# Kernel tuning notes

Hardware: AMD Instinct MI355X
Metric: run time of the kernel (lower is better)

Reference implementation:

```python
import jax, jax.numpy as jnp
import numpy as np
import math

D_MODEL = 1024
D_NEURON = 4 * D_MODEL
B, T = 2, 4096


def setup_inputs() -> dict:
    key = jax.random.key(0)
    ks = jax.random.split(key, 8)
    s = 1.0 / math.sqrt(D_MODEL)
    so = 1.0 / math.sqrt(D_NEURON)
    x = jax.random.normal(ks[0], (B, T, D_MODEL), dtype=jnp.float32)
    W_main = jax.random.uniform(ks[1], (D_NEURON, D_MODEL), jnp.float32, -s, s)
    W_gate = jax.random.uniform(ks[2], (D_NEURON, D_MODEL), jnp.float32, -s, s)
    W_mod = jax.random.uniform(ks[3], (D_NEURON, D_MODEL), jnp.float32, -s, s)
    W_out = jax.random.uniform(ks[4], (D_MODEL, D_NEURON), jnp.float32, -so, so)
    W_delta = jax.random.uniform(ks[5], (D_NEURON, D_MODEL), jnp.float32, -s, s)
    b_delta = jnp.full((D_NEURON,), -3.0, dtype=jnp.float32)
    # S4-style init: A_log = linspace(log(0.001), log(0.1), d_neuron)
    A_log = jnp.linspace(math.log(0.001), math.log(0.1), D_NEURON).astype(jnp.float32)
    sw_logit = jnp.zeros((D_NEURON,), dtype=jnp.float32)  # inv_sigmoid(0.5) = 0
    state = jnp.zeros((B, D_NEURON), dtype=jnp.float32)
    return {"x": x, "state": state, "W_main": W_main, "W_gate": W_gate,
            "W_mod": W_mod, "W_out": W_out, "W_delta": W_delta,
            "b_delta": b_delta, "A_log": A_log, "sw_logit": sw_logit}


def reference(x, state, W_main, W_gate, W_mod, W_out, W_delta, b_delta, A_log, sw_logit):
    # x: [B,T,Dm]; all projections to d_neuron Dn = 4*Dm
    raw = jnp.einsum('btm,nm->btn', x, W_main)            # [B,T,Dn]
    gate = jax.nn.sigmoid(jnp.einsum('btm,nm->btn', x, W_gate))
    mod = jnp.tanh(jnp.einsum('btm,nm->btn', x, W_mod))
    delta = jax.nn.softplus(jnp.einsum('btm,nm->btn', x, W_delta) + b_delta)
    A = -jnp.exp(A_log)                                   # [Dn]
    decay_t = jnp.exp(delta * A)                          # [B,T,Dn]
    update = (1.0 - decay_t) * gate * jnp.tanh(raw)       # [B,T,Dn]

    def step(s, du):
        d, u = du
        s = d * s + u
        return s, s

    # scan over time axis; carry [B,Dn]
    final_state, all_states = jax.lax.scan(
        step, state,
        (jnp.swapaxes(decay_t, 0, 1), jnp.swapaxes(update, 0, 1)))
    all_states = jnp.swapaxes(all_states, 0, 1)           # [B,T,Dn]

    sw = jax.nn.sigmoid(sw_logit)
    mixed = (1.0 - sw) * jax.nn.gelu(raw, approximate=False) + sw * all_states
    out = jnp.einsum('btn,mn->btm', mixed * (1.0 + mod), W_out)  # [B,T,Dm]
    return out, jax.lax.stop_gradient(final_state)
```

## Files before the change

### kernel.cpp

```cpp
#include <hip/hip_runtime.h>
#include <hip/hip_bf16.h>
#include <stdint.h>

#define DM 1024
#define DN 4096
#define BB 2
#define TT 4096
#define MR (BB*TT)
#define TC 512
#define NTC (TT/TC)
#define CR (BB*TC)
#define CN ((size_t)CR*DN)
#define SCH 16

typedef unsigned short u16;
typedef __attribute__((ext_vector_type(8))) short bf16x8;
typedef __attribute__((ext_vector_type(4))) float f32x4;

__device__ __forceinline__ float bf2f(u16 u) {
    unsigned int x = ((unsigned int)u) << 16; float f; __builtin_memcpy(&f, &x, 4); return f;
}
__device__ __forceinline__ u16 f2bf(float f) {
    __hip_bfloat16 h = __float2bfloat16(f); u16 u; __builtin_memcpy(&u, &h, 2); return u;
}
__device__ __forceinline__ float tanh_fast(float x) {
    float e = __expf(2.f * x);
    return 1.f - 2.f / (e + 1.f);
}
__device__ __forceinline__ float erf_fast(float x) {
    float ax = fabsf(x);
    float t = 1.f / (1.f + 0.3275911f * ax);
    float y = t * (0.254829592f + t * (-0.284496736f + t * (1.421413741f +
              t * (-1.453152027f + t * 1.061405429f))));
    float r = 1.f - y * __expf(-ax * ax);
    return copysignf(r, x);
}
__device__ __forceinline__ void async16(const void* g, void* l) {
    __builtin_amdgcn_global_load_lds(
        (const __attribute__((address_space(1))) void*)(uintptr_t)g,
        (__attribute__((address_space(3))) void*)(uint32_t)(uintptr_t)l,
        16, 0, 0);
}

__global__ void cvt7_kernel(const float4* __restrict__ x,
                            const float4* __restrict__ w0, const float4* __restrict__ w1,
                            const float4* __restrict__ w2, const float4* __restrict__ w3,
                            const float4* __restrict__ wo, const float4* __restrict__ st,
                            ushort4* __restrict__ xb, ushort4* __restrict__ w4b,
                            ushort4* __restrict__ woutb, float4* __restrict__ state_cur)
{
    const int XQ = (MR * DM) / 4;
    const int WQ = (DN * DM) / 4;
    const int SQ = XQ + 5 * WQ;
    int i = blockIdx.x * 256 + threadIdx.x;
    if (i >= SQ) {
        int j = i - SQ;
        if (j < (BB * DN) / 4) state_cur[j] = st[j];
        return;
    }
    const float4* s; ushort4* d;
    if (i < XQ) { s = x + i; d = xb + i; }
    else {
        int j = i - XQ;
        int seg = j >> 20;
        int off = j & (WQ - 1);
        if (seg < 4) {
            const float4* ws = (seg == 0) ? w0 : (seg == 1) ? w1 : (seg == 2) ? w2 : w3;
            s = ws + off; d = w4b + j;
        } else {
            s = wo + off; d = woutb + off;
        }
    }
    float4 v = *s;
    ushort4 o; o.x = f2bf(v.x); o.y = f2bf(v.y); o.z = f2bf(v.z); o.w = f2bf(v.w);
    *d = o;
}

#define BM 128
#define BN 128
#define BK 64

__global__ __launch_bounds__(256, 4) void gemm4_kernel(
    const u16* __restrict__ Xb,
    const u16* __restrict__ W4b,
    u16* __restrict__ raw_o, u16* __restrict__ sig_o,
    u16* __restrict__ modp_o, u16* __restrict__ omd_o,
    const float* __restrict__ A_log, const float* __restrict__ b_delta, int ci)
{
    const int bid = blockIdx.x;
    const int xcd = bid & 7;
    const int g = bid >> 3;
    const int m_idx = g & 7;
    const int pair = xcd * 16 + (g >> 3);
    const int n_idx = pair & 31;
    const int w = pair >> 5;

    const u16* Wp = W4b + (size_t)w * DN * DM;
    u16* Op = (w == 0) ? raw_o : (w == 1) ? sig_o : (w == 2) ? modp_o : omd_o;
    const int n0 = n_idx * BN;
    const int m0 = m_idx * BM;

    alignas(16) __shared__ u16 As[BM * BK];
    alignas(16) __shared__ u16 Bs[BN * BK];

    const int tid = threadIdx.x;
    const int lane = tid & 63;
    const int wave = tid >> 6;
    const int wm = (wave >> 1) * 64;
    const int wn = (wave & 1) * 64;
    const int l16 = lane & 15;
    const int quad = lane >> 4;
    const int sr8 = lane >> 3;
    const int cl = lane & 7;

    const f32x4 z4 = {0.f, 0.f, 0.f, 0.f};
    f32x4 acc[4][4];
#pragma unroll
    for (int i = 0; i < 4; i++)
#pragma unroll
        for (int j = 0; j < 4; j++) acc[i][j] = z4;

    for (int kt = 0; kt < DM; kt += BK) {
        __syncthreads();
#pragma unroll
        for (int it = 0; it < 4; ++it) {
            const int r = wave * 32 + it * 8 + sr8;
            const int cg = cl ^ (r & 7);
            async16(Wp + (size_t)(n0 + r) * DM + kt + cg * 8,
                    Bs + (wave * 32 + it * 8) * BK);
            const int lr = m0 + r;
            const int xrow = ((lr >> 9) << 12) + ci * TC + (lr & (TC - 1));
            async16(Xb + (size_t)xrow * DM + kt + cg * 8,
                    As + (wave * 32 + it * 8) * BK);
        }
        __syncthreads();
#pragma unroll
        for (int ks = 0; ks < BK; ks += 32) {
            bf16x8 af[4], bfr[4];
#pragma unroll
            for (int i = 0; i < 4; i++) {
                const int r = wm + i * 16 + l16;
                const int ch = ((ks >> 3) + quad) ^ (r & 7);
                af[i] = *(const bf16x8*)(As + r * BK + ch * 8);
            }
#pragma unroll
            for (int j = 0; j < 4; j++) {
                const int r = wn + j * 16 + l16;
                const int ch = ((ks >> 3) + quad) ^ (r & 7);
                bfr[j] = *(const bf16x8*)(Bs + r * BK + ch * 8);
            }
#pragma unroll
            for (int i = 0; i < 4; i++)
#pragma unroll
                for (int j = 0; j < 4; j++)
                    acc[i][j] = __builtin_amdgcn_mfma_f32_16x16x32_bf16(af[i], bfr[j], acc[i][j], 0, 0, 0);
        }
    }

    float Aj[4], bdj[4];
    if (w == 3) {
#pragma unroll
        for (int j = 0; j < 4; j++) {
            int n = n0 + wn + j * 16 + l16;
            Aj[j] = __expf(A_log[n]);
            bdj[j] = b_delta[n];
        }
    }

#pragma unroll
    for (int i = 0; i < 4; i++) {
#pragma unroll
        for (int j = 0; j < 4; j++) {
            int n = n0 + wn + j * 16 + l16;
#pragma unroll
            for (int r = 0; r < 4; r++) {
                int m = m0 + wm + i * 16 + quad * 4 + r;
                float z = acc[i][j][r];
                float o;
                if (w == 0) {
                    o = z;
                } else if (w == 1) {
                    o = 1.f / (1.f + __expf(-z));
                } else if (w == 2) {
                    o = 1.f + tanh_fast(z);
                } else {
                    float v = z + bdj[j];
                    float sp = fmaxf(v, 0.f) + __logf(1.f + __expf(-fabsf(v)));
                    o = 1.f - __expf(-Aj[j] * sp);
                }
                Op[(size_t)m * DN + n] = f2bf(o);
            }
        }
    }
}

__global__ __launch_bounds__(256, 4) void gemm_out_kernel(
    const u16* __restrict__ Zb, const u16* __restrict__ Wob, float* __restrict__ Out)
{
    const int bid = blockIdx.x;
    const int xcd = bid & 7;
    const int g = bid >> 3;
    const int n_idx = g & 7;
    const int m_idx = xcd * 8 + (g >> 3);
    const int n0 = n_idx * BN;
    const int m0 = m_idx * BM;

    alignas(16) __shared__ u16 As[BM * BK];
    alignas(16) __shared__ u16 Bs[BN * BK];

    const int tid = threadIdx.x;
    const int lane = tid & 63;
    const int wave = tid >> 6;
    const int wm = (wave >> 1) * 64;
    const int wn = (wave & 1) * 64;
    const int l16 = lane & 15;
    const int quad = lane >> 4;
    const int sr8 = lane >> 3;
    const int cl = lane & 7;

    const f32x4 z4 = {0.f, 0.f, 0.f, 0.f};
    f32x4 acc[4][4];
#pragma unroll
    for (int i = 0; i < 4; i++)
#pragma unroll
        for (int j = 0; j < 4; j++) acc[i][j] = z4;

    for (int kt = 0; kt < DN; kt += BK) {
        __syncthreads();
#pragma unroll
        for (int it = 0; it < 4; ++it) {
            const int r = wave * 32 + it * 8 + sr8;
            const int cg = cl ^ (r & 7);
            async16(Zb + (size_t)(m0 + r) * DN + kt + cg * 8,
                    As + (wave * 32 + it * 8) * BK);
            async16(Wob + (size_t)(n0 + r) * DN + kt + cg * 8,
                    Bs + (wave * 32 + it * 8) * BK);
        }
        __syncthreads();
#pragma unroll
        for (int ks = 0; ks < BK; ks += 32) {
            bf16x8 af[4], bfr[4];
#pragma unroll
            for (int i = 0; i < 4; i++) {
                const int r = wm + i * 16 + l16;
                const int ch = ((ks >> 3) + quad) ^ (r & 7);
                af[i] = *(const bf16x8*)(As + r * BK + ch * 8);
            }
#pragma unroll
            for (int j = 0; j < 4; j++) {
                const int r = wn + j * 16 + l16;
                const int ch = ((ks >> 3) + quad) ^ (r & 7);
                bfr[j] = *(const bf16x8*)(Bs + r * BK + ch * 8);
            }
#pragma unroll
            for (int i = 0; i < 4; i++)
#pragma unroll
                for (int j = 0; j < 4; j++)
                    acc[i][j] = __builtin_amdgcn_mfma_f32_16x16x32_bf16(af[i], bfr[j], acc[i][j], 0, 0, 0);
        }
    }

#pragma unroll
    for (int i = 0; i < 4; i++)
#pragma unroll
        for (int j = 0; j < 4; j++) {
            int n = n0 + wn + j * 16 + l16;
#pragma unroll
            for (int r = 0; r < 4; r++) {
                int m = m0 + wm + i * 16 + quad * 4 + r;
                Out[(size_t)m * DM + n] = acc[i][j][r];
            }
        }
}

__global__ __launch_bounds__(1024) void scan_fused(
    const u16* __restrict__ omd_a, const u16* __restrict__ sig_a,
    const u16* __restrict__ raw_a, const u16* __restrict__ modp_a,
    float* __restrict__ state_cur, const float* __restrict__ sw_logit,
    u16* __restrict__ Z, float* __restrict__ fs_out, int ci_t)
{
    __shared__ float Ds[32][32];
    __shared__ float Ss[32][32];
    __shared__ float Is[32][32];

    const int tid = threadIdx.x;
    const int nl = tid & 31;
    const int tg = tid >> 5;
    const int bx = blockIdx.x;
    const int nsl = bx & 127;
    const int b = bx >> 7;
    const int n = nsl * 32 + nl;

    const size_t base = ((size_t)(b * TC + tg * SCH)) * DN + n;

    const float sw = 1.f / (1.f + __expf(-sw_logit[n]));
    const float osw = 1.f - sw;

    float dv[SCH], uv[SCH], yv[SCH], mswv[SCH];

    float D = 1.f, s = 0.f;
#pragma unroll
    for (int t = 0; t < SCH; t++) {
        size_t idx = base + (size_t)t * DN;
        float omd = bf2f(omd_a[idx]);
        float sg = bf2f(sig_a[idx]);
        float rw = bf2f(raw_a[idx]);
        float mp = bf2f(modp_a[idx]);
        float d = 1.f - omd;
        float u = omd * sg * tanh_fast(rw);
        float g2 = 0.5f * rw * (1.f + erf_fast(rw * 0.70710678f));
        dv[t] = d; uv[t] = u;
        yv[t] = mp * osw * g2;
        mswv[t] = mp * sw;
        D *= d;
        s = d * s + u;
    }
    Ds[tg][nl] = D;
    Ss[tg][nl] = s;
    __syncthreads();

    if (tg == 0) {
        float si = state_cur[b * DN + n];
        Is[0][nl] = si;
        for (int c = 0; c < 31; c++) {
            si = Ds[c][nl] * si + Ss[c][nl];
            Is[c + 1][nl] = si;
        }
    }
    __syncthreads();

    float s2 = Is[tg][nl];
    const size_t gbase = ((size_t)(b * TT + ci_t * TC + tg * SCH)) * DN + n;
#pragma unroll
    for (int t = 0; t < SCH; t++) {
        s2 = dv[t] * s2 + uv[t];
        Z[gbase + (size_t)t * DN] = f2bf(yv[t] + mswv[t] * s2);
    }
    if (tg == 31) {
        state_cur[b * DN + n] = s2;
        if (ci_t == NTC - 1) fs_out[b * DN + n] = s2;
    }
}

extern "C" void kernel_launch(void* const* d_in, const int* in_sizes, int n_in,
                              void* d_out, int out_size, void* d_ws, size_t ws_size,
                              hipStream_t stream)
{
    const float* x = (const float*)d_in[0];
    const float* state = (const float*)d_in[1];
    const float* W_main = (const float*)d_in[2];
    const float* W_gate = (const float*)d_in[3];
    const float* W_mod = (const float*)d_in[4];
    const float* W_out = (const float*)d_in[5];
    const float* W_delta = (const float*)d_in[6];
    const float* b_delta = (const float*)d_in[7];
    const float* A_log = (const float*)d_in[8];
    const float* sw_logit = (const float*)d_in[9];

    float* out = (float*)d_out;
    float* fs_out = out + (size_t)MR * DM;

    const size_t NM = (size_t)MR * DN;
    u16* Zb = (u16*)d_ws;
    u16* raw_c = Zb + NM;
    u16* sig_c = raw_c + CN;
    u16* modp_c = sig_c + CN;
    u16* omd_c = modp_c + CN;
    u16* W4b = omd_c + CN;
    u16* xb = W4b + (size_t)4 * DN * DM;
    u16* woutb = xb + (size_t)MR * DM;
    float* state_cur = (float*)(woutb + (size_t)DM * DN);

    {
        const int total4 = (MR * DM) / 4 + 5 * ((DN * DM) / 4) + (BB * DN) / 4;
        cvt7_kernel<<<(total4 + 255) / 256, 256, 0, stream>>>(
            (const float4*)x, (const float4*)W_main, (const float4*)W_gate,
            (const float4*)W_mod, (const float4*)W_delta, (const float4*)W_out,
            (const float4*)state,
            (ushort4*)xb, (ushort4*)W4b, (ushort4*)woutb, (float4*)state_cur);
    }

    for (int ci = 0; ci < NTC; ci++) {
        gemm4_kernel<<<1024, 256, 0, stream>>>(xb, W4b, raw_c, sig_c, modp_c, omd_c,
                                               A_log, b_delta, ci);
        scan_fused<<<BB * (DN / 32), 1024, 0, stream>>>(omd_c, sig_c, raw_c, modp_c,
                                                        state_cur, sw_logit,
                                                        Zb, fs_out, ci);
    }

    gemm_out_kernel<<<512, 256, 0, stream>>>(Zb, woutb, out);
}
```

Baseline: 723.1 us.

## Rewrite projection GEMM as 256x256 tile, 8-wave, double-buffered phased pipeline

Replaces the 128x128 single-buffered projection GEMM with a 256x256 tile kernel using 8 waves and double-buffered LDS. Global loads for future K-tiles are issued in quarter steps interleaved with the MFMA phases, with explicit vmcnt waits, barriers and setprio. The goal is to hide load latency and raise operand reuse per tile. In exchange the grid shrinks to 256 blocks, which may leave CUs idle, and it needs 128KB of dynamic LDS plus a larger accumulator register footprint.

```diff
diff --git a/kernel.cpp b/kernel.cpp
--- a/kernel.cpp
+++ b/kernel.cpp
@@ -80,102 +80,169 @@
 #define BN 128
 #define BK 64
 
-__global__ __launch_bounds__(256, 4) void gemm4_kernel(
+
+#define G4_BM 256
+#define G4_BN 256
+#define G4_BK 64
+#define G4_NT (DM/G4_BK)
+#define G4_TSZ (G4_BM*G4_BK)
+
+__device__ __forceinline__ void stage_half_B(const u16* __restrict__ Wp, u16* lds_tile,
+                                             int n0, int r0, int kt, int tid)
+{
+    const int lane = tid & 63;
+    const int wv = tid >> 6;
+#pragma unroll
+    for (int l = 0; l < 2; ++l) {
+        const int r = r0 + (wv * 2 + l) * 8 + (lane >> 3);
+        const int cg = (lane & 7) ^ (r & 7);
+        async16(Wp + (size_t)(n0 + r) * DM + kt + cg * 8,
+                lds_tile + (size_t)(r0 + (wv * 2 + l) * 8) * G4_BK);
+    }
+}
+
+__device__ __forceinline__ void stage_half_A(const u16* __restrict__ Xb, u16* lds_tile,
+                                             int m0, int r0, int kt, int ci, int tid)
+{
+    const int lane = tid & 63;
+    const int wv = tid >> 6;
+#pragma unroll
+    for (int l = 0; l < 2; ++l) {
+        const int r = r0 + (wv * 2 + l) * 8 + (lane >> 3);
+        const int cg = (lane & 7) ^ (r & 7);
+        const int lr = m0 + r;
+        const int xrow = ((lr >> 9) << 12) + ci * TC + (lr & (TC - 1));
+        async16(Xb + (size_t)xrow * DM + kt + cg * 8,
+                lds_tile + (size_t)(r0 + (wv * 2 + l) * 8) * G4_BK);
+    }
+}
+
+#define PHASE_BODY(Q, STAGE_STMT, VMCNT_STMT)                                       \
+  {                                                                                 \
+    bf16x8 af[4][2];                                                                \
+    _Pragma("unroll")                                                               \
+    for (int i_ = 0; i_ < 4; ++i_) {                                                \
+      const int row_ = (Q) * 64 + i_ * 16 + l16;                                    \
+      const int rx_ = row_ & 7;                                                     \
+      af[i_][0] = *(const bf16x8*)(As_c + row_ * G4_BK + ((quad ^ rx_) * 8));       \
+      af[i_][1] = *(const bf16x8*)(As_c + row_ * G4_BK + (((4 + quad) ^ rx_) * 8)); \
+    }                                                                               \
+    STAGE_STMT                                                                      \
+    VMCNT_STMT                                                                      \
+    __builtin_amdgcn_s_barrier();                                                   \
+    asm volatile("s_waitcnt lgkmcnt(0)" ::: "memory");                              \
+    __builtin_amdgcn_sched_barrier(0);                                              \
+    __builtin_amdgcn_s_setprio(1);                                                  \
+    _Pragma("unroll")                                                               \
+    for (int i_ = 0; i_ < 4; ++i_) {                                                \
+      _Pragma("unroll")                                                             \
+      for (int j_ = 0; j_ < 2; ++j_) {                                              \
+        acc[(Q) * 4 + i_][j_] = __builtin_amdgcn_mfma_f32_16x16x32_bf16(            \
+            af[i_][0], bf[j_][0], acc[(Q) * 4 + i_][j_], 0, 0, 0);                  \
+        acc[(Q) * 4 + i_][j_] = __builtin_amdgcn_mfma_f32_16x16x32_bf16(            \
+            af[i_][1], bf[j_][1], acc[(Q) * 4 + i_][j_], 0, 0, 0);                  \
+      }                                                                             \
+    }                                                                               \
+    __builtin_amdgcn_s_setprio(0);                                                  \
+    __builtin_amdgcn_sched_barrier(0);                                              \
+    __builtin_amdgcn_s_barrier();                                                   \
+  }
+
+__global__ __launch_bounds__(512, 2) void gemm4_8ph(
     const u16* __restrict__ Xb,
     const u16* __restrict__ W4b,
     u16* __restrict__ raw_o, u16* __restrict__ sig_o,
     u16* __restrict__ modp_o, u16* __restrict__ omd_o,
     const float* __restrict__ A_log, const float* __restrict__ b_delta, int ci)
 {
+    extern __shared__ u16 lds[];
+    u16* const As0 = lds;
+    u16* const Bs0 = lds + G4_TSZ;
+    u16* const As1 = lds + 2 * G4_TSZ;
+    u16* const Bs1 = lds + 3 * G4_TSZ;
+
     const int bid = blockIdx.x;
     const int xcd = bid & 7;
     const int g = bid >> 3;
-    const int m_idx = g & 7;
-    const int pair = xcd * 16 + (g >> 3);
-    const int n_idx = pair & 31;
-    const int w = pair >> 5;
-
-    const u16* Wp = W4b + (size_t)w * DN * DM;
-    u16* Op = (w == 0) ? raw_o : (w == 1) ? sig_o : (w == 2) ? modp_o : omd_o;
-    const int n0 = n_idx * BN;
-    const int m0 = m_idx * BM;
-
-    alignas(16) __shared__ u16 As[BM * BK];
-    alignas(16) __shared__ u16 Bs[BN * BK];
+    const int m_idx = g & 3;
+    const int pair = xcd * 8 + (g >> 2);
+    const int n_idx = pair & 15;
+    const int w = pair >> 4;
+
+    const u16* __restrict__ Wp = W4b + (size_t)w * DN * DM;
+    u16* __restrict__ Op = (w == 0) ? raw_o : (w == 1) ? sig_o : (w == 2) ? modp_o : omd_o;
+    const int n0 = n_idx * G4_BN;
+    const int m0 = m_idx * G4_BM;
 
     const int tid = threadIdx.x;
     const int lane = tid & 63;
-    const int wave = tid >> 6;
-    const int wm = (wave >> 1) * 64;
-    const int wn = (wave & 1) * 64;
+    const int wv = tid >> 6;
     const int l16 = lane & 15;
     const int quad = lane >> 4;
-    const int sr8 = lane >> 3;
-    const int cl = lane & 7;
 
     const f32x4 z4 = {0.f, 0.f, 0.f, 0.f};
-    f32x4 acc[4][4];
-#pragma unroll
-    for (int i = 0; i < 4; i++)
-#pragma unroll
-        for (int j = 0; j < 4; j++) acc[i][j] = z4;
-
-    for (int kt = 0; kt < DM; kt += BK) {
-        __syncthreads();
-#pragma unroll
-        for (int it = 0; it < 4; ++it) {
-            const int r = wave * 32 + it * 8 + sr8;
-            const int cg = cl ^ (r & 7);
-            async16(Wp + (size_t)(n0 + r) * DM + kt + cg * 8,
-                    Bs + (wave * 32 + it * 8) * BK);
-            const int lr = m0 + r;
-            const int xrow = ((lr >> 9) << 12) + ci * TC + (lr & (TC - 1));
-            async16(Xb + (size_t)xrow * DM + kt + cg * 8,
-                    As + (wave * 32 + it * 8) * BK);
-        }
-        __syncthreads();
-#pragma unroll
-        for (int ks = 0; ks < BK; ks += 32) {
-            bf16x8 af[4], bfr[4];
-#pragma unroll
-            for (int i = 0; i < 4; i++) {
-                const int r = wm + i * 16 + l16;
-                const int ch = ((ks >> 3) + quad) ^ (r & 7);
-                af[i] = *(const bf16x8*)(As + r * BK + ch * 8);
-            }
-#pragma unroll
-            for (int j = 0; j < 4; j++) {
-                const int r = wn + j * 16 + l16;
-                const int ch = ((ks >> 3) + quad) ^ (r & 7);
-                bfr[j] = *(const bf16x8*)(Bs + r * BK + ch * 8);
-            }
-#pragma unroll
-            for (int i = 0; i < 4; i++)
-#pragma unroll
-                for (int j = 0; j < 4; j++)
-                    acc[i][j] = __builtin_amdgcn_mfma_f32_16x16x32_bf16(af[i], bfr[j], acc[i][j], 0, 0, 0);
-        }
-    }
-
-    float Aj[4], bdj[4];
+    f32x4 acc[16][2];
+#pragma unroll
+    for (int i = 0; i < 16; ++i) { acc[i][0] = z4; acc[i][1] = z4; }
+
+    stage_half_B(Wp, Bs0, n0, 0,   0, tid);
+    stage_half_B(Wp, Bs0, n0, 128, 0, tid);
+    stage_half_A(Xb, As0, m0, 0,   0, ci, tid);
+    stage_half_A(Xb, As0, m0, 128, 0, ci, tid);
+    stage_half_B(Wp, Bs1, n0, 0,   G4_BK, tid);
+    stage_half_B(Wp, Bs1, n0, 128, G4_BK, tid);
+    stage_half_A(Xb, As1, m0, 0,   G4_BK, ci, tid);
+    asm volatile("s_waitcnt vmcnt(6)" ::: "memory");
+    __builtin_amdgcn_s_barrier();
+
+    for (int t = 0; t < G4_NT; ++t) {
+        u16* const As_c = (t & 1) ? As1 : As0;
+        u16* const Bs_c = (t & 1) ? Bs1 : Bs0;
+        u16* const As_n = (t & 1) ? As0 : As1;
+
+        bf16x8 bf[2][2];
+#pragma unroll
+        for (int j = 0; j < 2; ++j) {
+            const int row = wv * 32 + j * 16 + l16;
+            const int rx = row & 7;
+            bf[j][0] = *(const bf16x8*)(Bs_c + row * G4_BK + ((quad ^ rx) * 8));
+            bf[j][1] = *(const bf16x8*)(Bs_c + row * G4_BK + (((4 + quad) ^ rx) * 8));
+        }
+
+        PHASE_BODY(0,
+            if (t + 1 < G4_NT) stage_half_A(Xb, As_n, m0, 128, (t + 1) * G4_BK, ci, tid); ,
+            )
+        PHASE_BODY(1,
+            if (t + 2 < G4_NT) stage_half_B(Wp, Bs_c, n0, 0, (t + 2) * G4_BK, tid); ,
+            )
+        PHASE_BODY(2,
+            if (t + 2 < G4_NT) stage_half_B(Wp, Bs_c, n0, 128, (t + 2) * G4_BK, tid); ,
+            )
+        PHASE_BODY(3,
+            if (t + 2 < G4_NT) stage_half_A(Xb, As_c, m0, 0, (t + 2) * G4_BK, ci, tid); ,
+            if (t < G4_NT - 2) { asm volatile("s_waitcnt vmcnt(6)" ::: "memory"); }
+            else               { asm volatile("s_waitcnt vmcnt(0)" ::: "memory"); } )
+    }
+
+    float Aj[2], bdj[2];
     if (w == 3) {
 #pragma unroll
-        for (int j = 0; j < 4; j++) {
-            int n = n0 + wn + j * 16 + l16;
+        for (int j = 0; j < 2; ++j) {
+            int n = n0 + wv * 32 + j * 16 + l16;
             Aj[j] = __expf(A_log[n]);
             bdj[j] = b_delta[n];
         }
     }
 
 #pragma unroll
-    for (int i = 0; i < 4; i++) {
-#pragma unroll
-        for (int j = 0; j < 4; j++) {
-            int n = n0 + wn + j * 16 + l16;
-#pragma unroll
-            for (int r = 0; r < 4; r++) {
-                int m = m0 + wm + i * 16 + quad * 4 + r;
-                float z = acc[i][j][r];
+    for (int f = 0; f < 16; ++f) {
+#pragma unroll
+        for (int j = 0; j < 2; ++j) {
+            const int n = n0 + wv * 32 + j * 16 + l16;
+#pragma unroll
+            for (int r = 0; r < 4; ++r) {
+                const int m = m0 + f * 16 + quad * 4 + r;
+                float z = acc[f][j][r];
                 float o;
                 if (w == 0) {
                     o = z;
@@ -371,6 +438,14 @@
     u16* woutb = xb + (size_t)MR * DM;
     float* state_cur = (float*)(woutb + (size_t)DM * DN);
 
+    static bool attr_set = false;
+    if (!attr_set) {
+        (void)hipFuncSetAttribute((const void*)gemm4_8ph,
+                                  hipFuncAttributeMaxDynamicSharedMemorySize,
+                                  4 * G4_TSZ * (int)sizeof(u16));
+        attr_set = true;
+    }
+
     {
         const int total4 = (MR * DM) / 4 + 5 * ((DN * DM) / 4) + (BB * DN) / 4;
         cvt7_kernel<<<(total4 + 255) / 256, 256, 0, stream>>>(
@@ -381,8 +456,8 @@
     }
 
     for (int ci = 0; ci < NTC; ci++) {
-        gemm4_kernel<<<1024, 256, 0, stream>>>(xb, W4b, raw_c, sig_c, modp_c, omd_c,
-                                               A_log, b_delta, ci);
+        gemm4_8ph<<<256, 512, 4 * G4_TSZ * sizeof(u16), stream>>>(
+            xb, W4b, raw_c, sig_c, modp_c, omd_c, A_log, b_delta, ci);
         scan_fused<<<BB * (DN / 32), 1024, 0, stream>>>(omd_c, sig_c, raw_c, modp_c,
                                                         state_cur, sw_logit,
                                                         Zb, fs_out, ci);
```

New measurement: 759.5 us. 1.05x slower.

## Vectorize scan kernel with 8-wide bf16 loads and recompute in second pass

Applied to the files above, without the earlier changes.

Restructures the chunked scan so each thread handles 8 adjacent neurons over 8 timesteps using 16-byte bf16x8 loads and stores instead of scalar 2-byte accesses. Per-thread register arrays are replaced by re-reading inputs in the second pass and recomputing decay and update, which trades extra global/L2 reads and math for fewer registers. Block size drops from 1024 to 256 threads and the inter-chunk prefix scan now walks 64 segments serially per neuron, making that serial section longer.

```diff
diff --git a/kernel.cpp b/kernel.cpp
--- a/kernel.cpp
+++ b/kernel.cpp
@@ -11,7 +11,7 @@
 #define NTC (TT/TC)
 #define CR (BB*TC)
 #define CN ((size_t)CR*DN)
-#define SCH 16
+#define SC2 8
 
 typedef unsigned short u16;
 typedef __attribute__((ext_vector_type(8))) short bf16x8;
@@ -273,72 +273,97 @@
         }
 }
 
-__global__ __launch_bounds__(1024) void scan_fused(
+__global__ __launch_bounds__(256) void scan_fused(
     const u16* __restrict__ omd_a, const u16* __restrict__ sig_a,
     const u16* __restrict__ raw_a, const u16* __restrict__ modp_a,
     float* __restrict__ state_cur, const float* __restrict__ sw_logit,
     u16* __restrict__ Z, float* __restrict__ fs_out, int ci_t)
 {
-    __shared__ float Ds[32][32];
-    __shared__ float Ss[32][32];
-    __shared__ float Is[32][32];
+    __shared__ float Ds[64][32];
+    __shared__ float Ss[64][32];
+    __shared__ float Is[64][32];
 
     const int tid = threadIdx.x;
-    const int nl = tid & 31;
-    const int tg = tid >> 5;
+    const int ng = tid & 3;
+    const int tg = tid >> 2;
     const int bx = blockIdx.x;
     const int nsl = bx & 127;
     const int b = bx >> 7;
-    const int n = nsl * 32 + nl;
-
-    const size_t base = ((size_t)(b * TC + tg * SCH)) * DN + n;
-
-    const float sw = 1.f / (1.f + __expf(-sw_logit[n]));
-    const float osw = 1.f - sw;
-
-    float dv[SCH], uv[SCH], yv[SCH], mswv[SCH];
-
-    float D = 1.f, s = 0.f;
-#pragma unroll
-    for (int t = 0; t < SCH; t++) {
+    const int n0 = nsl * 32 + ng * 8;
+    const int nb = ng * 8;
+
+    float sw8[8], osw8[8];
+#pragma unroll
+    for (int k = 0; k < 8; k++) {
+        float sw = 1.f / (1.f + __expf(-sw_logit[n0 + k]));
+        sw8[k] = sw; osw8[k] = 1.f - sw;
+    }
+
+    const size_t base = ((size_t)(b * TC + tg * SC2)) * DN + n0;
+
+    float D[8], S[8];
+#pragma unroll
+    for (int k = 0; k < 8; k++) { D[k] = 1.f; S[k] = 0.f; }
+#pragma unroll
+    for (int t = 0; t < SC2; t++) {
         size_t idx = base + (size_t)t * DN;
-        float omd = bf2f(omd_a[idx]);
-        float sg = bf2f(sig_a[idx]);
-        float rw = bf2f(raw_a[idx]);
-        float mp = bf2f(modp_a[idx]);
-        float d = 1.f - omd;
-        float u = omd * sg * tanh_fast(rw);
-        float g2 = 0.5f * rw * (1.f + erf_fast(rw * 0.70710678f));
-        dv[t] = d; uv[t] = u;
-        yv[t] = mp * osw * g2;
-        mswv[t] = mp * sw;
-        D *= d;
-        s = d * s + u;
-    }
-    Ds[tg][nl] = D;
-    Ss[tg][nl] = s;
+        bf16x8 o8 = *(const bf16x8*)(omd_a + idx);
+        bf16x8 g8 = *(const bf16x8*)(sig_a + idx);
+        bf16x8 r8 = *(const bf16x8*)(raw_a + idx);
+#pragma unroll
+        for (int k = 0; k < 8; k++) {
+            float omd = bf2f((u16)o8[k]);
+            float sg  = bf2f((u16)g8[k]);
+            float rw  = bf2f((u16)r8[k]);
+            float d = 1.f - omd;
+            float u = omd * sg * tanh_fast(rw);
+            D[k] *= d;
+            S[k] = d * S[k] + u;
+        }
+    }
+#pragma unroll
+    for (int k = 0; k < 8; k++) { Ds[tg][nb + k] = D[k]; Ss[tg][nb + k] = S[k]; }
     __syncthreads();
 
-    if (tg == 0) {
+    if (tid < 32) {
+        const int n = nsl * 32 + tid;
         float si = state_cur[b * DN + n];
-        Is[0][nl] = si;
-        for (int c = 0; c < 31; c++) {
-            si = Ds[c][nl] * si + Ss[c][nl];
-            Is[c + 1][nl] = si;
-        }
+#pragma unroll
+        for (int c = 0; c < 64; c++) {
+            Is[c][tid] = si;
+            si = Ds[c][tid] * si + Ss[c][tid];
+        }
+        state_cur[b * DN + n] = si;
+        if (ci_t == NTC - 1) fs_out[b * DN + n] = si;
     }
     __syncthreads();
 
-    float s2 = Is[tg][nl];
-    const size_t gbase = ((size_t)(b * TT + ci_t * TC + tg * SCH)) * DN + n;
-#pragma unroll
-    for (int t = 0; t < SCH; t++) {
-        s2 = dv[t] * s2 + uv[t];
-        Z[gbase + (size_t)t * DN] = f2bf(yv[t] + mswv[t] * s2);
-    }
-    if (tg == 31) {
-        state_cur[b * DN + n] = s2;
-        if (ci_t == NTC - 1) fs_out[b * DN + n] = s2;
+    float s2[8];
+#pragma unroll
+    for (int k = 0; k < 8; k++) s2[k] = Is[tg][nb + k];
+    const size_t gbase = ((size_t)(b * TT + ci_t * TC + tg * SC2)) * DN + n0;
+#pragma unroll
+    for (int t = 0; t < SC2; t++) {
+        size_t idx = base + (size_t)t * DN;
+        bf16x8 o8 = *(const bf16x8*)(omd_a + idx);
+        bf16x8 g8 = *(const bf16x8*)(sig_a + idx);
+        bf16x8 r8 = *(const bf16x8*)(raw_a + idx);
+        bf16x8 m8 = *(const bf16x8*)(modp_a + idx);
+        bf16x8 zv;
+#pragma unroll
+        for (int k = 0; k < 8; k++) {
+            float omd = bf2f((u16)o8[k]);
+            float sg  = bf2f((u16)g8[k]);
+            float rw  = bf2f((u16)r8[k]);
+            float mp  = bf2f((u16)m8[k]);
+            float d = 1.f - omd;
+            float u = omd * sg * tanh_fast(rw);
+            s2[k] = d * s2[k] + u;
+            float g2 = 0.5f * rw * (1.f + erf_fast(rw * 0.70710678f));
+            float z = mp * (osw8[k] * g2 + sw8[k] * s2[k]);
+            zv[k] = (short)f2bf(z);
+        }
+        *(bf16x8*)(Z + gbase + (size_t)t * DN) = zv;
     }
 }
 
@@ -383,9 +408,9 @@
     for (int ci = 0; ci < NTC; ci++) {
         gemm4_kernel<<<1024, 256, 0, stream>>>(xb, W4b, raw_c, sig_c, modp_c, omd_c,
                                                A_log, b_delta, ci);
-        scan_fused<<<BB * (DN / 32), 1024, 0, stream>>>(omd_c, sig_c, raw_c, modp_c,
-                                                        state_cur, sw_logit,
-                                                        Zb, fs_out, ci);
+        scan_fused<<<BB * (DN / 32), 256, 0, stream>>>(omd_c, sig_c, raw_c, modp_c,
+                                                       state_cur, sw_logit,
+                                                       Zb, fs_out, ci);
     }
 
     gemm_out_kernel<<<512, 256, 0, stream>>>(Zb, woutb, out);
```

Result: slower. 783.9 us (+8.4%).
